# Kernel tuning notes

Measured on AMD Instinct MI355X. Metric: run time of the kernel, lower is better.

## Reference

```python
import jax, jax.numpy as jnp
import numpy as np

B, S, D, E, F, K = 2, 1024, 2048, 8, 1024, 2


def setup_inputs() -> dict:
    key = jax.random.key(0)
    ks = jax.random.split(key, 5)
    s = 0.02  # init scale for weights
    return {
        "hidden_states": jax.random.normal(ks[0], (B, S, D), dtype=jnp.float32),
        "gate_w": jax.random.normal(ks[1], (E, D), dtype=jnp.float32) * s,
        "w_gate": jax.random.normal(ks[2], (E, D, F), dtype=jnp.float32) * s,
        "w_up": jax.random.normal(ks[3], (E, D, F), dtype=jnp.float32) * s,
        "w_down": jax.random.normal(ks[4], (E, F, D), dtype=jnp.float32) * s,
        "top_k": K,
    }


def reference(hidden_states, gate_w, w_gate, w_up, w_down, top_k):
    b, s, d = hidden_states.shape
    x = hidden_states.reshape(-1, d)                      # [T, D] tokens
    T = x.shape[0]
    n_exp = gate_w.shape[0]

    # router gate (bias-free linear) + topk softmax
    router_logits = jnp.einsum('td,ed->te', x, gate_w)    # [T, E]
    probs = jax.nn.softmax(router_logits, axis=-1)
    top_w, top_i = jax.lax.top_k(probs, top_k)            # [T, K]
    top_w = top_w / jnp.sum(top_w, axis=-1, keepdims=True)  # renormalize over selected experts

    # scatter routing weights into dense combine matrix [T, E] (zero for unselected experts)
    comb = jnp.zeros((T, n_exp), dtype=x.dtype)
    comb = comb.at[jnp.arange(T)[:, None], top_i].set(top_w)

    # SwiGLU expert MLPs, computed for all experts and masked by routing weights
    g = jax.nn.silu(jnp.einsum('td,edf->etf', x, w_gate))  # [E, T, F]
    u = jnp.einsum('td,edf->etf', x, w_up)                 # [E, T, F]
    h = (g * u) * comb.T[:, :, None]                       # weight before down-proj to fuse combine
    y = jnp.einsum('etf,efd->td', h, w_down)               # [T, D] combined output

    final = y.reshape(b, s, d)
    return final, router_logits
```

## Files before the change

kernel.cpp:

```cpp
#include <hip/hip_runtime.h>
#include <hip/hip_bf16.h>

#define T_TOK 2048
#define D_DIM 2048
#define N_EXP 8
#define F_DIM 1024

typedef __attribute__((ext_vector_type(8))) short short8;
typedef __attribute__((ext_vector_type(4))) float floatx4;

__device__ __forceinline__ short f2bf(float f) {
  union { float f; unsigned u; } v; v.f = f;
  unsigned r = v.u + 0x7fffu + ((v.u >> 16) & 1u);
  return (short)(r >> 16);
}

__device__ __forceinline__ floatx4 mfma16(short8 a, short8 b, floatx4 c) {
  return __builtin_amdgcn_mfma_f32_16x16x32_bf16(a, b, c, 0, 0, 0);
}

__device__ __forceinline__ void gload16(const void* g, void* l) {
  __builtin_amdgcn_global_load_lds(
      (const __attribute__((address_space(1))) unsigned int*)g,
      (__attribute__((address_space(3))) unsigned int*)l, 16, 0, 0);
}

__global__ __launch_bounds__(256) void pack_wgwu(const float* __restrict__ src,
                                                 short* __restrict__ dst) {
  int fb = blockIdx.x, s = blockIdx.y, e = blockIdx.z;
  __shared__ float tile[64][65];
  int tx = threadIdx.x & 63, ty = threadIdx.x >> 6;
  const float* sp = src + (size_t)e * D_DIM * F_DIM + (size_t)(s * 64) * F_DIM + fb * 64;
#pragma unroll
  for (int i = 0; i < 64; i += 4)
    tile[ty + i][tx] = sp[(size_t)(ty + i) * F_DIM + tx];
  __syncthreads();
  short* dp = dst + (size_t)((e * 16 + fb) * 32 + s) * 4096;
#pragma unroll
  for (int i = 0; i < 64; i += 4)
    dp[(ty + i) * 64 + tx] = f2bf(tile[tx][ty + i]);
}

__global__ __launch_bounds__(256) void pack_wd(const float* __restrict__ src,
                                               short* __restrict__ dst) {
  int nb = blockIdx.x, s = blockIdx.y, e = blockIdx.z;
  __shared__ float tile[64][129];
  int tx2 = threadIdx.x & 127, ty2 = threadIdx.x >> 7;
  const float* sp = src + (size_t)e * F_DIM * D_DIM + (size_t)(s * 64) * D_DIM + nb * 128;
#pragma unroll
  for (int i = 0; i < 64; i += 2)
    tile[ty2 + i][tx2] = sp[(size_t)(ty2 + i) * D_DIM + tx2];
  __syncthreads();
  int tx = threadIdx.x & 63, ty = threadIdx.x >> 6;
  short* dp = dst + (size_t)((e * 16 + nb) * 16 + s) * 8192;
#pragma unroll
  for (int r = 0; r < 128; r += 4)
    dp[(r + ty) * 64 + tx] = f2bf(tile[tx][r + ty]);
}

__global__ __launch_bounds__(256) void router_kernel(
    const float* __restrict__ x, const float* __restrict__ gate_w,
    short* __restrict__ x_bf, float* __restrict__ out_logits,
    int* __restrict__ counts, int* __restrict__ tok_ids, float* __restrict__ tok_wts) {
  int t = blockIdx.x;
  int tid = threadIdx.x;
  const float* xr = x + (size_t)t * D_DIM + tid * 8;
  floatx4 xv0 = *(const floatx4*)xr;
  floatx4 xv1 = *(const floatx4*)(xr + 4);
  float xs[8];
#pragma unroll
  for (int j = 0; j < 4; j++) { xs[j] = xv0[j]; xs[4 + j] = xv1[j]; }
  union { short8 v; short s[8]; } xb;
#pragma unroll
  for (int j = 0; j < 8; j++) xb.s[j] = f2bf(xs[j]);
  *(short8*)(x_bf + (size_t)t * D_DIM + tid * 8) = xb.v;

  float p[N_EXP];
#pragma unroll
  for (int e = 0; e < N_EXP; e++) {
    const float* gw = gate_w + (size_t)e * D_DIM + tid * 8;
    floatx4 g0 = *(const floatx4*)gw;
    floatx4 g1 = *(const floatx4*)(gw + 4);
    float s = 0.f;
#pragma unroll
    for (int j = 0; j < 4; j++) s += xs[j] * g0[j] + xs[4 + j] * g1[j];
    p[e] = s;
  }
  __shared__ float red[N_EXP * 4];
  __shared__ float slog[N_EXP];
  int lane = tid & 63, wv = tid >> 6;
#pragma unroll
  for (int e = 0; e < N_EXP; e++) {
    float v = p[e];
#pragma unroll
    for (int off = 32; off > 0; off >>= 1) v += __shfl_down(v, off);
    if (lane == 0) red[e * 4 + wv] = v;
  }
  __syncthreads();
  if (tid < N_EXP) {
    float s = red[tid * 4] + red[tid * 4 + 1] + red[tid * 4 + 2] + red[tid * 4 + 3];
    slog[tid] = s;
    out_logits[(size_t)t * N_EXP + tid] = s;
  }
  __syncthreads();
  if (tid == 0) {
    float l[N_EXP];
#pragma unroll
    for (int e = 0; e < N_EXP; e++) l[e] = slog[e];
    int e0 = 0;
#pragma unroll
    for (int e = 1; e < N_EXP; e++) if (l[e] > l[e0]) e0 = e;
    int e1 = (e0 == 0) ? 1 : 0;
#pragma unroll
    for (int e = 0; e < N_EXP; e++) if (e != e0 && l[e] > l[e1]) e1 = e;
    float p1 = __expf(l[e1] - l[e0]);
    float s = 1.f + p1;
    int pos0 = atomicAdd(&counts[e0], 1);
    tok_ids[e0 * T_TOK + pos0] = t;
    tok_wts[e0 * T_TOK + pos0] = 1.f / s;
    int pos1 = atomicAdd(&counts[e1], 1);
    tok_ids[e1 * T_TOK + pos1] = t | (1 << 16);
    tok_wts[e1 * T_TOK + pos1] = p1 / s;
  }
}

__global__ __launch_bounds__(256) void tok2row_kernel(
    const int* __restrict__ counts, const int* __restrict__ tok_ids,
    int* __restrict__ tok2row) {
  int tid = threadIdx.x;
  int base = 0;
  for (int e = 0; e < N_EXP; e++) {
    int c = counts[e];
    for (int pos = tid; pos < c; pos += 256) {
      int raw = tok_ids[e * T_TOK + pos];
      tok2row[(raw & 0xFFFF) * 2 + (raw >> 16)] = base + pos;
    }
    base += c;
  }
}

__global__ __launch_bounds__(256, 2) void gemm1_kernel(
    const short* __restrict__ x_bf,
    const short* __restrict__ pwg, const short* __restrict__ pwu,
    const int* __restrict__ counts, const int* __restrict__ tok_ids,
    const float* __restrict__ tok_wts,
    short* __restrict__ h_sorted) {
  int e = blockIdx.x >> 4;
  int mt = blockIdx.x & 15;
  int count = counts[e];
  if (mt * 128 >= count) return;
  int fb = blockIdx.y;
  int hb = 0;
#pragma unroll
  for (int i = 0; i < N_EXP; i++) { int c = counts[i]; if (i < e) hb += c; }

  __shared__ short sA[8192];
  __shared__ short sBg[4096];
  __shared__ short sBu[4096];
  __shared__ int s_tok[128];
  __shared__ float s_wt[128];

  int tid = threadIdx.x;
  if (tid < 128) {
    int r = mt * 128 + tid;
    if (r < count) { s_tok[tid] = tok_ids[e * T_TOK + r]; s_wt[tid] = tok_wts[e * T_TOK + r]; }
    else { s_tok[tid] = 0; s_wt[tid] = 0.f; }
  }
  __syncthreads();

  int lane = tid & 63, wv = tid >> 6;
  int wr = wv >> 1, wc = wv & 1;
  int l16 = lane & 15, qd = lane >> 4;
  int lr = lane >> 3, lc = lane & 7;
  int csw8 = (lc ^ lr) * 8;

  int offA[4], offB[2];
#pragma unroll
  for (int it = 0; it < 4; it++) {
    int r = wv * 32 + it * 8 + lr;
    offA[it] = (s_tok[r] & 0xFFFF) * D_DIM + csw8;
  }
#pragma unroll
  for (int it = 0; it < 2; it++)
    offB[it] = (wv * 16 + it * 8 + lr) * 64 + csw8;
  const short* pBg = pwg + (size_t)((e * 16 + fb) * 32) * 4096;
  const short* pBu = pwu + (size_t)((e * 16 + fb) * 32) * 4096;

  floatx4 accG[4][2] = {};
  floatx4 accU[4][2] = {};
  int sw = l16 & 7;
  const short* rA  = sA  + (wr * 64 + l16) * 64;
  const short* rBg = sBg + (wc * 32 + l16) * 64;
  const short* rBu = sBu + (wc * 32 + l16) * 64;

  for (int s = 0; s < D_DIM / 64; s++) {
    __syncthreads();
#pragma unroll
    for (int it = 0; it < 4; it++)
      gload16(x_bf + offA[it] + s * 64, sA + wv * 2048 + it * 512);
#pragma unroll
    for (int it = 0; it < 2; it++) {
      gload16(pBg + (size_t)s * 4096 + offB[it], sBg + wv * 1024 + it * 512);
      gload16(pBu + (size_t)s * 4096 + offB[it], sBu + wv * 1024 + it * 512);
    }
    __syncthreads();
#pragma unroll
    for (int kk = 0; kk < 2; kk++) {
      short8 a[4], bg[2], bu[2];
      int c = ((kk * 4 + qd) ^ sw) * 8;
#pragma unroll
      for (int mi = 0; mi < 4; mi++) a[mi] = *(const short8*)(rA + mi * 16 * 64 + c);
#pragma unroll
      for (int nj = 0; nj < 2; nj++) {
        bg[nj] = *(const short8*)(rBg + nj * 16 * 64 + c);
        bu[nj] = *(const short8*)(rBu + nj * 16 * 64 + c);
      }
#pragma unroll
      for (int mi = 0; mi < 4; mi++)
#pragma unroll
        for (int nj = 0; nj < 2; nj++) {
          accG[mi][nj] = mfma16(a[mi], bg[nj], accG[mi][nj]);
          accU[mi][nj] = mfma16(a[mi], bu[nj], accU[mi][nj]);
        }
    }
  }

#pragma unroll
  for (int mi = 0; mi < 4; mi++)
#pragma unroll
    for (int r = 0; r < 4; r++) {
      int rowl = wr * 64 + mi * 16 + qd * 4 + r;
      if (mt * 128 + rowl < count) {
        float wt = s_wt[rowl];
        short* hdst = h_sorted + (size_t)(hb + mt * 128 + rowl) * F_DIM
                    + fb * 64 + wc * 32 + l16;
#pragma unroll
        for (int nj = 0; nj < 2; nj++) {
          float g = accG[mi][nj][r], u = accU[mi][nj][r];
          float sg = g / (1.f + __expf(-g));
          hdst[nj * 16] = f2bf(sg * u * wt);
        }
      }
    }
}

__global__ __launch_bounds__(256, 2) void gemm2_kernel(
    const short* __restrict__ h_sorted, const short* __restrict__ pwd,
    const int* __restrict__ counts,
    float* __restrict__ y_sorted) {
  int e = blockIdx.x >> 4;
  int mt = blockIdx.x & 15;
  int count = counts[e];
  if (mt * 128 >= count) return;
  int nb = blockIdx.y;
  int hb = 0;
#pragma unroll
  for (int i = 0; i < N_EXP; i++) { int c = counts[i]; if (i < e) hb += c; }

  __shared__ short sA[8192];
  __shared__ short sB[8192];

  int tid = threadIdx.x;
  int lane = tid & 63, wv = tid >> 6;
  int wr = wv >> 1, wc = wv & 1;
  int l16 = lane & 15, qd = lane >> 4;
  int lr = lane >> 3, lc = lane & 7;
  int csw8 = (lc ^ lr) * 8;

  int offA[4], offB[4];
#pragma unroll
  for (int it = 0; it < 4; it++) {
    int r = wv * 32 + it * 8 + lr;
    offA[it] = (hb + mt * 128 + r) * F_DIM + csw8;
    offB[it] = r * 64 + csw8;
  }
  const short* pB = pwd + (size_t)((e * 16 + nb) * 16) * 8192;

  floatx4 acc[4][4] = {};
  int sw = l16 & 7;
  const short* rA = sA + (wr * 64 + l16) * 64;
  const short* rB = sB + (wc * 64 + l16) * 64;

  for (int s = 0; s < F_DIM / 64; s++) {
    __syncthreads();
#pragma unroll
    for (int it = 0; it < 4; it++) {
      gload16(h_sorted + offA[it] + s * 64, sA + wv * 2048 + it * 512);
      gload16(pB + (size_t)s * 8192 + offB[it], sB + wv * 2048 + it * 512);
    }
    __syncthreads();
#pragma unroll
    for (int kk = 0; kk < 2; kk++) {
      short8 a[4], b[4];
      int c = ((kk * 4 + qd) ^ sw) * 8;
#pragma unroll
      for (int mi = 0; mi < 4; mi++) a[mi] = *(const short8*)(rA + mi * 16 * 64 + c);
#pragma unroll
      for (int nj = 0; nj < 4; nj++) b[nj] = *(const short8*)(rB + nj * 16 * 64 + c);
#pragma unroll
      for (int mi = 0; mi < 4; mi++)
#pragma unroll
        for (int nj = 0; nj < 4; nj++)
          acc[mi][nj] = mfma16(a[mi], b[nj], acc[mi][nj]);
    }
  }

#pragma unroll
  for (int mi = 0; mi < 4; mi++)
#pragma unroll
    for (int r = 0; r < 4; r++) {
      int rowl = wr * 64 + mi * 16 + qd * 4 + r;
      if (mt * 128 + rowl < count) {
        float* dst = y_sorted + (size_t)(hb + mt * 128 + rowl) * D_DIM
                   + nb * 128 + wc * 64 + l16;
#pragma unroll
        for (int nj = 0; nj < 4; nj++)
          dst[nj * 16] = acc[mi][nj][r];
      }
    }
}

__global__ __launch_bounds__(256) void combine_kernel(
    const float* __restrict__ y_sorted, const int* __restrict__ tok2row,
    float* __restrict__ outY) {
  int t = blockIdx.x;
  int r0 = tok2row[t * 2], r1 = tok2row[t * 2 + 1];
  int i = threadIdx.x * 8;
  const floatx4* a = (const floatx4*)(y_sorted + (size_t)r0 * D_DIM + i);
  const floatx4* b = (const floatx4*)(y_sorted + (size_t)r1 * D_DIM + i);
  floatx4* o = (floatx4*)(outY + (size_t)t * D_DIM + i);
  o[0] = a[0] + b[0];
  o[1] = a[1] + b[1];
}

extern "C" void kernel_launch(void* const* d_in, const int* in_sizes, int n_in,
                              void* d_out, int out_size, void* d_ws, size_t ws_size,
                              hipStream_t stream) {
  (void)in_sizes; (void)n_in; (void)out_size; (void)ws_size;
  const float* hidden = (const float*)d_in[0];
  const float* gate_w = (const float*)d_in[1];
  const float* w_gate = (const float*)d_in[2];
  const float* w_up   = (const float*)d_in[3];
  const float* w_down = (const float*)d_in[4];
  float* out = (float*)d_out;
  float* outY = out;
  float* outLogits = out + (size_t)T_TOK * D_DIM;

  char* ws = (char*)d_ws;
  size_t off = 0;
  int* counts = (int*)(ws + off); off += 256;
  int* tok_ids = (int*)(ws + off); off += (size_t)N_EXP * T_TOK * 4;
  float* tok_wts = (float*)(ws + off); off += (size_t)N_EXP * T_TOK * 4;
  int* tok2row = (int*)(ws + off); off += (size_t)T_TOK * 2 * 4;
  short* x_bf = (short*)(ws + off); off += (size_t)T_TOK * D_DIM * 2;
  short* pwg = (short*)(ws + off); off += (size_t)N_EXP * F_DIM * D_DIM * 2;
  short* pwu = (short*)(ws + off); off += (size_t)N_EXP * F_DIM * D_DIM * 2;
  short* pwd = (short*)(ws + off); off += (size_t)N_EXP * D_DIM * F_DIM * 2;
  short* h_sorted = (short*)(ws + off); off += (size_t)T_TOK * 2 * F_DIM * 2;
  float* y_sorted = (float*)(ws + off); off += (size_t)T_TOK * 2 * D_DIM * 4;

  hipMemsetAsync(counts, 0, 256, stream);

  pack_wgwu<<<dim3(16, 32, N_EXP), 256, 0, stream>>>(w_gate, pwg);
  pack_wgwu<<<dim3(16, 32, N_EXP), 256, 0, stream>>>(w_up, pwu);
  pack_wd<<<dim3(16, 16, N_EXP), 256, 0, stream>>>(w_down, pwd);

  router_kernel<<<T_TOK, 256, 0, stream>>>(hidden, gate_w, x_bf, outLogits,
                                           counts, tok_ids, tok_wts);
  tok2row_kernel<<<1, 256, 0, stream>>>(counts, tok_ids, tok2row);

  gemm1_kernel<<<dim3(N_EXP * 16, F_DIM / 64), 256, 0, stream>>>(
      x_bf, pwg, pwu, counts, tok_ids, tok_wts, h_sorted);

  gemm2_kernel<<<dim3(N_EXP * 16, D_DIM / 128), 256, 0, stream>>>(
      h_sorted, pwd, counts, y_sorted);

  combine_kernel<<<T_TOK, 256, 0, stream>>>(y_sorted, tok2row, outY);
}
```

Baseline: 483.8 us.

## Double-buffer LDS tiles in expert GEMMs and interleave experts in grid order

Both expert GEMM kernels now keep two LDS buffers. The next K-slice is prefetched with global_load_lds while the MFMAs run on the current one, which leaves one barrier per iteration instead of two. The launch becomes 1D with the expert index varying fastest, so tiles from different experts are spread across CUs. The shared token-id and weight staging is replaced by direct global reads. LDS use per block doubles to 64KB, which may limit occupancy to two blocks per CU.

```diff
diff --git a/kernel.cpp b/kernel.cpp
--- a/kernel.cpp
+++ b/kernel.cpp
@@ -145,29 +145,21 @@
     const int* __restrict__ counts, const int* __restrict__ tok_ids,
     const float* __restrict__ tok_wts,
     short* __restrict__ h_sorted) {
-  int e = blockIdx.x >> 4;
-  int mt = blockIdx.x & 15;
+  int lin = blockIdx.x;
+  int e  = lin & 7;
+  int mt = (lin >> 3) & 15;
+  int fb = (lin >> 7) & 15;
   int count = counts[e];
   if (mt * 128 >= count) return;
-  int fb = blockIdx.y;
   int hb = 0;
 #pragma unroll
   for (int i = 0; i < N_EXP; i++) { int c = counts[i]; if (i < e) hb += c; }
 
-  __shared__ short sA[8192];
-  __shared__ short sBg[4096];
-  __shared__ short sBu[4096];
-  __shared__ int s_tok[128];
-  __shared__ float s_wt[128];
+  __shared__ short sA[2][8192];
+  __shared__ short sBg[2][4096];
+  __shared__ short sBu[2][4096];
 
   int tid = threadIdx.x;
-  if (tid < 128) {
-    int r = mt * 128 + tid;
-    if (r < count) { s_tok[tid] = tok_ids[e * T_TOK + r]; s_wt[tid] = tok_wts[e * T_TOK + r]; }
-    else { s_tok[tid] = 0; s_wt[tid] = 0.f; }
-  }
-  __syncthreads();
-
   int lane = tid & 63, wv = tid >> 6;
   int wr = wv >> 1, wc = wv & 1;
   int l16 = lane & 15, qd = lane >> 4;
@@ -178,7 +170,8 @@
 #pragma unroll
   for (int it = 0; it < 4; it++) {
     int r = wv * 32 + it * 8 + lr;
-    offA[it] = (s_tok[r] & 0xFFFF) * D_DIM + csw8;
+    int raw = (mt * 128 + r < count) ? tok_ids[e * T_TOK + mt * 128 + r] : 0;
+    offA[it] = (raw & 0xFFFF) * D_DIM + csw8;
   }
 #pragma unroll
   for (int it = 0; it < 2; it++)
@@ -189,21 +182,35 @@
   floatx4 accG[4][2] = {};
   floatx4 accU[4][2] = {};
   int sw = l16 & 7;
-  const short* rA  = sA  + (wr * 64 + l16) * 64;
-  const short* rBg = sBg + (wc * 32 + l16) * 64;
-  const short* rBu = sBu + (wc * 32 + l16) * 64;
-
+  int rAo  = (wr * 64 + l16) * 64;
+  int rBo  = (wc * 32 + l16) * 64;
+
+#pragma unroll
+  for (int it = 0; it < 4; it++)
+    gload16(x_bf + offA[it], &sA[0][wv * 2048 + it * 512]);
+#pragma unroll
+  for (int it = 0; it < 2; it++) {
+    gload16(pBg + offB[it], &sBg[0][wv * 1024 + it * 512]);
+    gload16(pBu + offB[it], &sBu[0][wv * 1024 + it * 512]);
+  }
+
+  int cur = 0;
   for (int s = 0; s < D_DIM / 64; s++) {
     __syncthreads();
-#pragma unroll
-    for (int it = 0; it < 4; it++)
-      gload16(x_bf + offA[it] + s * 64, sA + wv * 2048 + it * 512);
-#pragma unroll
-    for (int it = 0; it < 2; it++) {
-      gload16(pBg + (size_t)s * 4096 + offB[it], sBg + wv * 1024 + it * 512);
-      gload16(pBu + (size_t)s * 4096 + offB[it], sBu + wv * 1024 + it * 512);
-    }
-    __syncthreads();
+    if (s + 1 < D_DIM / 64) {
+      int nxt = cur ^ 1;
+#pragma unroll
+      for (int it = 0; it < 4; it++)
+        gload16(x_bf + offA[it] + (s + 1) * 64, &sA[nxt][wv * 2048 + it * 512]);
+#pragma unroll
+      for (int it = 0; it < 2; it++) {
+        gload16(pBg + (size_t)(s + 1) * 4096 + offB[it], &sBg[nxt][wv * 1024 + it * 512]);
+        gload16(pBu + (size_t)(s + 1) * 4096 + offB[it], &sBu[nxt][wv * 1024 + it * 512]);
+      }
+    }
+    const short* rA  = &sA[cur][rAo];
+    const short* rBg = &sBg[cur][rBo];
+    const short* rBu = &sBu[cur][rBo];
 #pragma unroll
     for (int kk = 0; kk < 2; kk++) {
       short8 a[4], bg[2], bu[2];
@@ -223,6 +230,7 @@
           accU[mi][nj] = mfma16(a[mi], bu[nj], accU[mi][nj]);
         }
     }
+    cur ^= 1;
   }
 
 #pragma unroll
@@ -231,7 +239,7 @@
     for (int r = 0; r < 4; r++) {
       int rowl = wr * 64 + mi * 16 + qd * 4 + r;
       if (mt * 128 + rowl < count) {
-        float wt = s_wt[rowl];
+        float wt = tok_wts[e * T_TOK + mt * 128 + rowl];
         short* hdst = h_sorted + (size_t)(hb + mt * 128 + rowl) * F_DIM
                     + fb * 64 + wc * 32 + l16;
 #pragma unroll
@@ -248,17 +256,18 @@
     const short* __restrict__ h_sorted, const short* __restrict__ pwd,
     const int* __restrict__ counts,
     float* __restrict__ y_sorted) {
-  int e = blockIdx.x >> 4;
-  int mt = blockIdx.x & 15;
+  int lin = blockIdx.x;
+  int e  = lin & 7;
+  int mt = (lin >> 3) & 15;
+  int nb = (lin >> 7) & 15;
   int count = counts[e];
   if (mt * 128 >= count) return;
-  int nb = blockIdx.y;
   int hb = 0;
 #pragma unroll
   for (int i = 0; i < N_EXP; i++) { int c = counts[i]; if (i < e) hb += c; }
 
-  __shared__ short sA[8192];
-  __shared__ short sB[8192];
+  __shared__ short sA[2][8192];
+  __shared__ short sB[2][8192];
 
   int tid = threadIdx.x;
   int lane = tid & 63, wv = tid >> 6;
@@ -278,17 +287,28 @@
 
   floatx4 acc[4][4] = {};
   int sw = l16 & 7;
-  const short* rA = sA + (wr * 64 + l16) * 64;
-  const short* rB = sB + (wc * 64 + l16) * 64;
-
+  int rAo = (wr * 64 + l16) * 64;
+  int rBo = (wc * 64 + l16) * 64;
+
+#pragma unroll
+  for (int it = 0; it < 4; it++) {
+    gload16(h_sorted + offA[it], &sA[0][wv * 2048 + it * 512]);
+    gload16(pB + offB[it], &sB[0][wv * 2048 + it * 512]);
+  }
+
+  int cur = 0;
   for (int s = 0; s < F_DIM / 64; s++) {
     __syncthreads();
-#pragma unroll
-    for (int it = 0; it < 4; it++) {
-      gload16(h_sorted + offA[it] + s * 64, sA + wv * 2048 + it * 512);
-      gload16(pB + (size_t)s * 8192 + offB[it], sB + wv * 2048 + it * 512);
-    }
-    __syncthreads();
+    if (s + 1 < F_DIM / 64) {
+      int nxt = cur ^ 1;
+#pragma unroll
+      for (int it = 0; it < 4; it++) {
+        gload16(h_sorted + offA[it] + (s + 1) * 64, &sA[nxt][wv * 2048 + it * 512]);
+        gload16(pB + (size_t)(s + 1) * 8192 + offB[it], &sB[nxt][wv * 2048 + it * 512]);
+      }
+    }
+    const short* rA = &sA[cur][rAo];
+    const short* rB = &sB[cur][rBo];
 #pragma unroll
     for (int kk = 0; kk < 2; kk++) {
       short8 a[4], b[4];
@@ -303,6 +323,7 @@
         for (int nj = 0; nj < 4; nj++)
           acc[mi][nj] = mfma16(a[mi], b[nj], acc[mi][nj]);
     }
+    cur ^= 1;
   }
 
 #pragma unroll
@@ -369,10 +390,10 @@
                                            counts, tok_ids, tok_wts);
   tok2row_kernel<<<1, 256, 0, stream>>>(counts, tok_ids, tok2row);
 
-  gemm1_kernel<<<dim3(N_EXP * 16, F_DIM / 64), 256, 0, stream>>>(
+  gemm1_kernel<<<dim3(N_EXP * 16 * 16), 256, 0, stream>>>(
       x_bf, pwg, pwu, counts, tok_ids, tok_wts, h_sorted);
 
-  gemm2_kernel<<<dim3(N_EXP * 16, D_DIM / 128), 256, 0, stream>>>(
+  gemm2_kernel<<<dim3(N_EXP * 16 * 16), 256, 0, stream>>>(
       h_sorted, pwd, counts, y_sorted);
 
   combine_kernel<<<T_TOK, 256, 0, stream>>>(y_sorted, tok2row, outY);
```

New measurement: 447.6 us. 7.5% less time.
